# Optimization experiments

Hardware: AMD Instinct MI355X
Metric: run time of the kernel (lower is better)

Reference implementation:

```python
import jax, jax.numpy as jnp
import numpy as np

FORCE = 8.0
N_STATE = 40
BATCH = 524288


def setup_inputs() -> dict:
    key = jax.random.key(0)
    x0 = jax.random.normal(key, (BATCH, N_STATE), dtype=jnp.float32)
    t = jnp.float32(0.0)          # unused: system is autonomous (torch code passes nan)
    dt = jnp.float32(0.05)        # canonical Lorenz96 RK4 step
    return {"x0": x0, "t": t, "dt": dt}


def _dxdt(x):
    # torch shift(x, n) == roll(x, -n, dims=-1)
    # dxdt = (shift(x,1) - shift(x,-2)) * shift(x,-1) - x + force
    return (jnp.roll(x, -1, axis=-1) - jnp.roll(x, 2, axis=-1)) * jnp.roll(x, 1, axis=-1) - x + FORCE


def reference(x0, t, dt):
    # Classic RK4 step (rk4_torch); t is ignored (autonomous RHS).
    k1 = _dxdt(x0)
    k2 = _dxdt(x0 + 0.5 * dt * k1)
    k3 = _dxdt(x0 + 0.5 * dt * k2)
    k4 = _dxdt(x0 + dt * k3)
    return x0 + (dt / 6.0) * (k1 + 2.0 * k2 + 2.0 * k3 + k4)
```

## Files before the change

### kernel.cpp

```cpp
#include <hip/hip_runtime.h>


#define FORCE 8.0f

typedef float f32x4 __attribute__((ext_vector_type(4)));

__device__ __forceinline__ void nt_store(float4* p, const float4& v) {
    __builtin_nontemporal_store(*(const f32x4*)&v, (f32x4*)p);
}

__device__ __forceinline__ float4 rk4_chunk(const float4 vm2, const float4 vm1,
                                            const float4 v0,  const float4 vp1,
                                            const float dt,   const float hdt)
{
    float xa[16];
    xa[0]=vm2.x;  xa[1]=vm2.y;  xa[2]=vm2.z;  xa[3]=vm2.w;
    xa[4]=vm1.x;  xa[5]=vm1.y;  xa[6]=vm1.z;  xa[7]=vm1.w;
    xa[8]=v0.x;   xa[9]=v0.y;   xa[10]=v0.z;  xa[11]=v0.w;
    xa[12]=vp1.x; xa[13]=vp1.y; xa[14]=vp1.z; xa[15]=vp1.w;

    float k1[13], y1[13];
#pragma unroll
    for (int i = 0; i < 13; ++i)
        k1[i] = fmaf(xa[i+3] - xa[i], xa[i+1], FORCE - xa[i+2]);
#pragma unroll
    for (int i = 0; i < 13; ++i)
        y1[i] = fmaf(hdt, k1[i], xa[i+2]);

    float k2[10], y2[10];
#pragma unroll
    for (int i = 0; i < 10; ++i)
        k2[i] = fmaf(y1[i+3] - y1[i], y1[i+1], FORCE - y1[i+2]);
#pragma unroll
    for (int i = 0; i < 10; ++i)
        y2[i] = fmaf(hdt, k2[i], xa[i+4]);

    float k3[7], y3[7];
#pragma unroll
    for (int i = 0; i < 7; ++i)
        k3[i] = fmaf(y2[i+3] - y2[i], y2[i+1], FORCE - y2[i+2]);
#pragma unroll
    for (int i = 0; i < 7; ++i)
        y3[i] = fmaf(dt, k3[i], xa[i+6]);

    float k4[4];
#pragma unroll
    for (int i = 0; i < 4; ++i)
        k4[i] = fmaf(y3[i+3] - y3[i], y3[i+1], FORCE - y3[i+2]);

    const float sc = dt * (1.0f / 6.0f);
    float4 r;
    float t0 = k1[6] + k4[0]; t0 = fmaf(2.0f, k2[4], t0); t0 = fmaf(2.0f, k3[2], t0);
    float t1 = k1[7] + k4[1]; t1 = fmaf(2.0f, k2[5], t1); t1 = fmaf(2.0f, k3[3], t1);
    float t2 = k1[8] + k4[2]; t2 = fmaf(2.0f, k2[6], t2); t2 = fmaf(2.0f, k3[4], t2);
    float t3 = k1[9] + k4[3]; t3 = fmaf(2.0f, k2[7], t3); t3 = fmaf(2.0f, k3[5], t3);
    r.x = fmaf(sc, t0, xa[8]);
    r.y = fmaf(sc, t1, xa[9]);
    r.z = fmaf(sc, t2, xa[10]);
    r.w = fmaf(sc, t3, xa[11]);
    return r;
}

__global__ __launch_bounds__(320)
void lorenz96_rk4_lds(const float4* __restrict__ x0,
                      const float* __restrict__ dt_p,
                      float4* __restrict__ out)
{
    __shared__ float4 tile[320];

    const unsigned tid = threadIdx.x;
    const unsigned f   = blockIdx.x * 320u + tid;

    const float4 own = x0[f];
    tile[tid] = own;

    const float dt  = dt_p[0];
    const float hdt = 0.5f * dt;

    const unsigned c   = tid % 10u;
    const unsigned rb  = tid - c;
    const unsigned im2 = rb + ((c >= 2u) ? c - 2u : c + 8u);
    const unsigned im1 = rb + ((c >= 1u) ? c - 1u : c + 9u);
    const unsigned ip1 = rb + ((c <= 8u) ? c + 1u : c - 9u);

    __syncthreads();

    const float4 vm2 = tile[im2];
    const float4 vm1 = tile[im1];
    const float4 vp1 = tile[ip1];

    const float4 r = rk4_chunk(vm2, vm1, own, vp1, dt, hdt);
    nt_store(&out[f], r);
}

__global__ __launch_bounds__(256)
void lorenz96_rk4_halo(const float4* __restrict__ x0,
                       const float* __restrict__ dt_p,
                       float4* __restrict__ out,
                       long nf4)
{
    const long f = (long)blockIdx.x * blockDim.x + threadIdx.x;
    if (f >= nf4) return;
    const long r  = f / 10;
    const int  c  = (int)(f - r * 10);
    const long rb = r * 10;
    const int cm2 = (c >= 2) ? c - 2 : c + 8;
    const int cm1 = (c >= 1) ? c - 1 : c + 9;
    const int cp1 = (c <= 8) ? c + 1 : c - 9;

    const float4 vm2 = x0[rb + cm2];
    const float4 vm1 = x0[rb + cm1];
    const float4 v0  = x0[rb + c  ];
    const float4 vp1 = x0[rb + cp1];

    const float dt  = dt_p[0];
    const float hdt = 0.5f * dt;
    const float4 res = rk4_chunk(vm2, vm1, v0, vp1, dt, hdt);
    nt_store(&out[f], res);
}

extern "C" void kernel_launch(void* const* d_in, const int* in_sizes, int n_in,
                              void* d_out, int out_size, void* d_ws, size_t ws_size,
                              hipStream_t stream) {
    const float4* x0 = (const float4*)d_in[0];
    const float* dt = (const float*)d_in[2];
    float4* out = (float4*)d_out;

    const long nf4 = (long)in_sizes[0] / 4;

    if (nf4 % 320 == 0) {
        const unsigned grid = (unsigned)(nf4 / 320);
        lorenz96_rk4_lds<<<dim3(grid), dim3(320), 0, stream>>>(x0, dt, out);
    } else {
        const int block = 256;
        const long grid = (nf4 + block - 1) / block;
        lorenz96_rk4_halo<<<dim3((unsigned)grid), dim3(block), 0, stream>>>(
            x0, dt, out, nf4);
    }
}
```

Measured before the change: 147.2 us.

## Process 8-float chunks per thread with pipelined persistent-style loop over groups

Replaces the LDS-based one-float4-per-thread kernel with a fixed 2048-block grid where each thread handles five 8-float chunks, loading halos directly from global memory and double-buffering the next chunk's loads while computing the current one. Wider chunks reduce redundant halo recomputation per output, and the interleaving aims to hide memory latency. It adds redundant global halo reads (served mostly by cache) and higher register pressure, and the fast path applies only when the size matches exactly five strides.

```diff
diff --git a/kernel.cpp b/kernel.cpp
--- a/kernel.cpp
+++ b/kernel.cpp
@@ -9,9 +9,141 @@
     __builtin_nontemporal_store(*(const f32x4*)&v, (f32x4*)p);
 }
 
-__device__ __forceinline__ float4 rk4_chunk(const float4 vm2, const float4 vm1,
-                                            const float4 v0,  const float4 vp1,
-                                            const float dt,   const float hdt)
+struct f4x2 { float4 a, b; };
+
+__device__ __forceinline__ f4x2 rk4_chunk8(const float4 w0, const float4 w1,
+                                           const float4 w2, const float4 w3,
+                                           const float4 w4,
+                                           const float dt, const float hdt)
+{
+    float xa[20];
+    xa[0]=w0.x;  xa[1]=w0.y;  xa[2]=w0.z;  xa[3]=w0.w;
+    xa[4]=w1.x;  xa[5]=w1.y;  xa[6]=w1.z;  xa[7]=w1.w;
+    xa[8]=w2.x;  xa[9]=w2.y;  xa[10]=w2.z; xa[11]=w2.w;
+    xa[12]=w3.x; xa[13]=w3.y; xa[14]=w3.z; xa[15]=w3.w;
+    xa[16]=w4.x; xa[17]=w4.y; xa[18]=w4.z; xa[19]=w4.w;
+
+    float k1[17], y1[17];
+#pragma unroll
+    for (int i = 0; i < 17; ++i)
+        k1[i] = fmaf(xa[i+3] - xa[i], xa[i+1], FORCE - xa[i+2]);
+#pragma unroll
+    for (int i = 0; i < 17; ++i)
+        y1[i] = fmaf(hdt, k1[i], xa[i+2]);
+
+    float k2[14], y2[14];
+#pragma unroll
+    for (int i = 0; i < 14; ++i)
+        k2[i] = fmaf(y1[i+3] - y1[i], y1[i+1], FORCE - y1[i+2]);
+#pragma unroll
+    for (int i = 0; i < 14; ++i)
+        y2[i] = fmaf(hdt, k2[i], xa[i+4]);
+
+    float k3[11], y3[11];
+#pragma unroll
+    for (int i = 0; i < 11; ++i)
+        k3[i] = fmaf(y2[i+3] - y2[i], y2[i+1], FORCE - y2[i+2]);
+#pragma unroll
+    for (int i = 0; i < 11; ++i)
+        y3[i] = fmaf(dt, k3[i], xa[i+6]);
+
+    float k4[8];
+#pragma unroll
+    for (int i = 0; i < 8; ++i)
+        k4[i] = fmaf(y3[i+3] - y3[i], y3[i+1], FORCE - y3[i+2]);
+
+    const float sc = dt * (1.0f / 6.0f);
+    float o[8];
+#pragma unroll
+    for (int m = 0; m < 8; ++m) {
+        float t = k1[m+6] + k4[m];
+        t = fmaf(2.0f, k2[m+4], t);
+        t = fmaf(2.0f, k3[m+2], t);
+        o[m] = fmaf(sc, t, xa[8+m]);
+    }
+    f4x2 r;
+    r.a = make_float4(o[0], o[1], o[2], o[3]);
+    r.b = make_float4(o[4], o[5], o[6], o[7]);
+    return r;
+}
+
+#define LOADS8(G, CP, W0, W1, W2, W3, W4)                                    \
+    {                                                                        \
+        const unsigned rb  = 2u * ((G) - (CP));                              \
+        const unsigned two = 2u * (CP);                                      \
+        const unsigned cm2 = ((CP) == 0u) ? 8u : two - 2u;                   \
+        const unsigned cm1 = ((CP) == 0u) ? 9u : two - 1u;                   \
+        const unsigned cp2 = ((CP) == 4u) ? 0u : two + 2u;                   \
+        W0 = x0[rb + cm2];                                                   \
+        W1 = x0[rb + cm1];                                                   \
+        W2 = x0[rb + two];                                                   \
+        W3 = x0[rb + two + 1u];                                              \
+        W4 = x0[rb + cp2];                                                   \
+    }
+
+#define STORE8(G, R)                                                         \
+    {                                                                        \
+        nt_store(&out[2u * (G)],      R.a);                                  \
+        nt_store(&out[2u * (G) + 1u], R.b);                                  \
+    }
+
+__global__ __launch_bounds__(256)
+void lorenz96_rk4_fat8(const float4* __restrict__ x0,
+                       const float* __restrict__ dt_p,
+                       float4* __restrict__ out,
+                       unsigned stride)
+{
+    const unsigned tid = blockIdx.x * blockDim.x + threadIdx.x;
+    const float dt  = dt_p[0];
+    const float hdt = 0.5f * dt;
+
+    unsigned g0 = tid;
+    unsigned c0 = tid % 5u;
+    unsigned g1 = g0 + stride;
+    unsigned c1 = c0 + 3u; if (c1 >= 5u) c1 -= 5u;
+
+    float4 A0, A1, A2, A3, A4;
+    float4 B0, B1, B2, B3, B4;
+    LOADS8(g0, c0, A0, A1, A2, A3, A4)
+    LOADS8(g1, c1, B0, B1, B2, B3, B4)
+
+    f4x2 r0 = rk4_chunk8(A0, A1, A2, A3, A4, dt, hdt);
+    STORE8(g0, r0)
+    {
+        const unsigned g2 = g1 + stride;
+        unsigned c2 = c1 + 3u; if (c2 >= 5u) c2 -= 5u;
+        LOADS8(g2, c2, A0, A1, A2, A3, A4)
+        g0 = g2; c0 = c2;
+    }
+
+    f4x2 r1 = rk4_chunk8(B0, B1, B2, B3, B4, dt, hdt);
+    STORE8(g1, r1)
+    {
+        const unsigned g3 = g0 + stride;
+        unsigned c3 = c0 + 3u; if (c3 >= 5u) c3 -= 5u;
+        LOADS8(g3, c3, B0, B1, B2, B3, B4)
+        g1 = g3; c1 = c3;
+    }
+
+    f4x2 r2 = rk4_chunk8(A0, A1, A2, A3, A4, dt, hdt);
+    STORE8(g0, r2)
+    {
+        const unsigned g4 = g1 + stride;
+        unsigned c4 = c1 + 3u; if (c4 >= 5u) c4 -= 5u;
+        LOADS8(g4, c4, A0, A1, A2, A3, A4)
+        g0 = g4; c0 = c4;
+    }
+
+    f4x2 r3 = rk4_chunk8(B0, B1, B2, B3, B4, dt, hdt);
+    STORE8(g1, r3)
+
+    f4x2 r4 = rk4_chunk8(A0, A1, A2, A3, A4, dt, hdt);
+    STORE8(g0, r4)
+}
+
+__device__ __forceinline__ float4 rk4_chunk4(const float4 vm2, const float4 vm1,
+                                             const float4 v0,  const float4 vp1,
+                                             const float dt,   const float hdt)
 {
     float xa[16];
     xa[0]=vm2.x;  xa[1]=vm2.y;  xa[2]=vm2.z;  xa[3]=vm2.w;
@@ -61,38 +193,6 @@
     return r;
 }
 
-__global__ __launch_bounds__(320)
-void lorenz96_rk4_lds(const float4* __restrict__ x0,
-                      const float* __restrict__ dt_p,
-                      float4* __restrict__ out)
-{
-    __shared__ float4 tile[320];
-
-    const unsigned tid = threadIdx.x;
-    const unsigned f   = blockIdx.x * 320u + tid;
-
-    const float4 own = x0[f];
-    tile[tid] = own;
-
-    const float dt  = dt_p[0];
-    const float hdt = 0.5f * dt;
-
-    const unsigned c   = tid % 10u;
-    const unsigned rb  = tid - c;
-    const unsigned im2 = rb + ((c >= 2u) ? c - 2u : c + 8u);
-    const unsigned im1 = rb + ((c >= 1u) ? c - 1u : c + 9u);
-    const unsigned ip1 = rb + ((c <= 8u) ? c + 1u : c - 9u);
-
-    __syncthreads();
-
-    const float4 vm2 = tile[im2];
-    const float4 vm1 = tile[im1];
-    const float4 vp1 = tile[ip1];
-
-    const float4 r = rk4_chunk(vm2, vm1, own, vp1, dt, hdt);
-    nt_store(&out[f], r);
-}
-
 __global__ __launch_bounds__(256)
 void lorenz96_rk4_halo(const float4* __restrict__ x0,
                        const float* __restrict__ dt_p,
@@ -115,7 +215,7 @@
 
     const float dt  = dt_p[0];
     const float hdt = 0.5f * dt;
-    const float4 res = rk4_chunk(vm2, vm1, v0, vp1, dt, hdt);
+    const float4 res = rk4_chunk4(vm2, vm1, v0, vp1, dt, hdt);
     nt_store(&out[f], res);
 }
 
@@ -127,14 +227,17 @@
     float4* out = (float4*)d_out;
 
     const long nf4 = (long)in_sizes[0] / 4;
-
-    if (nf4 % 320 == 0) {
-        const unsigned grid = (unsigned)(nf4 / 320);
-        lorenz96_rk4_lds<<<dim3(grid), dim3(320), 0, stream>>>(x0, dt, out);
+    const int block = 256;
+    const unsigned grid = 2048;
+    const unsigned stride = grid * (unsigned)block;
+
+    const long nf8 = nf4 / 2;
+    if (nf4 % 2 == 0 && (unsigned long)nf8 == 5ul * stride) {
+        lorenz96_rk4_fat8<<<dim3(grid), dim3(block), 0, stream>>>(
+            x0, dt, out, stride);
     } else {
-        const int block = 256;
-        const long grid = (nf4 + block - 1) / block;
-        lorenz96_rk4_halo<<<dim3((unsigned)grid), dim3(block), 0, stream>>>(
+        const long g = (nf4 + block - 1) / block;
+        lorenz96_rk4_halo<<<dim3((unsigned)g), dim3(block), 0, stream>>>(
             x0, dt, out, nf4);
     }
 }
```

Result: slower. 161.6 us (+9.8%).
